# Optimization experiments

Hardware: AMD Instinct MI355X
Metric: run time of the kernel (lower is better)

## Reference

```python
import jax, jax.numpy as jnp
import numpy as np

CAPACITY_FACTOR = 2  # GShard top-2 gating: C = 2*S/E


def setup_inputs() -> dict:
    key = jax.random.key(0)
    k1, k2, k3, k4 = jax.random.split(key, 4)
    B, T, M, E, F = 4, 1024, 1024, 8, 4096
    x = jax.random.normal(k1, (B, T, M), dtype=jnp.float32)
    wg = jax.random.normal(k2, (M, E), dtype=jnp.float32) * 0.02
    w1 = jax.random.normal(k3, (E, M, F), dtype=jnp.float32) * 0.02
    w2 = jax.random.normal(k4, (E, F, M), dtype=jnp.float32) * 0.02
    return {"x": x, "wg": wg, "w1": w1, "w2": w2}


def top2_gate(xs, wg):
    # xs: [S, M] tokens; wg: [M, E] gate projection.
    S = xs.shape[0]
    E = wg.shape[1]
    C = CAPACITY_FACTOR * S // E  # expert capacity
    logits = xs @ wg                                  # [S, E]
    gates = jax.nn.softmax(logits, axis=-1)           # [S, E]
    # top-1 expert
    idx1 = jnp.argmax(gates, axis=-1)                 # [S]
    mask1 = jax.nn.one_hot(idx1, E, dtype=jnp.int32)  # [S, E]
    # top-2 expert: mask out top-1 and take argmax again
    logits_no1 = jnp.where(mask1.astype(bool), -jnp.inf, logits)
    idx2 = jnp.argmax(logits_no1, axis=-1)
    mask2 = jax.nn.one_hot(idx2, E, dtype=jnp.int32)
    # positions within each expert's buffer (cumsum over tokens)
    loc1 = jnp.cumsum(mask1, axis=0) - 1              # [S, E]
    loc2 = jnp.cumsum(mask2, axis=0) - 1 + jnp.sum(mask1, axis=0, keepdims=True)
    # load-balancing auxiliary loss
    me = jnp.mean(gates, axis=0)
    ce = jnp.mean(mask1.astype(gates.dtype), axis=0)
    l_aux = jnp.mean(me * ce) * (E * E)
    # drop tokens beyond capacity
    mask1 = mask1 * (loc1 < C)
    mask2 = mask2 * (loc2 < C)
    loc1_s = jnp.sum(loc1 * mask1, axis=1)            # [S] slot of token in its top-1 expert
    loc2_s = jnp.sum(loc2 * mask2, axis=1)
    mask1f = mask1.astype(gates.dtype)
    mask2f = mask2.astype(gates.dtype)
    gates1_s = jnp.sum(gates * mask1f, axis=1)
    gates2_s = jnp.sum(gates * mask2f, axis=1)
    denom = gates1_s + gates2_s
    denom = jnp.where(denom < 1e-9, 1e-9, denom)
    g1 = gates1_s / denom
    g2 = gates2_s / denom
    # combine weights [S, E, C]
    combine = (g1[:, None] * mask1f)[:, :, None] * jax.nn.one_hot(loc1_s, C, dtype=gates.dtype)[:, None, :] \
            + (g2[:, None] * mask2f)[:, :, None] * jax.nn.one_hot(loc2_s, C, dtype=gates.dtype)[:, None, :]
    dispatch = (combine > 0).astype(gates.dtype)      # one-hot dispatch mask [S, E, C]
    return l_aux, combine, dispatch


def reference(x, wg, w1, w2):
    B, T, M = x.shape
    xs = x.reshape(-1, M)                                  # [S, M]
    l_aux, combine_weights, dispatch_mask = top2_gate(xs, wg)
    # dispatch: one-hot matmul (E*C x S) @ (S x M) -> [E, C, M]
    dispatched = jnp.einsum('sec,sm->ecm', dispatch_mask, xs)
    # per-expert FFN (relu)
    h = jax.nn.relu(jnp.einsum('ecm,emf->ecf', dispatched, w1))
    expert_out = jnp.einsum('ecf,efm->ecm', h, w2)         # [E, C, M]
    # combine: (S x E*C) @ (E*C x M) -> [S, M]
    combined = jnp.einsum('sec,ecm->sm', combine_weights, expert_out)
    return combined.reshape(B, T, M), l_aux
```

## Files before the change

### kernel.cpp

```cpp
#include <hip/hip_runtime.h>
#include <hip/hip_bf16.h>

typedef unsigned short u16;
typedef short bf16x8 __attribute__((ext_vector_type(8)));
typedef float f32x4 __attribute__((ext_vector_type(4)));
typedef u16 u16x8 __attribute__((ext_vector_type(8)));
typedef u16 u16x4 __attribute__((ext_vector_type(4)));

#define S_TOK 4096
#define MDIM 1024
#define EDIM 8
#define FDIM 4096
#define CCAP 1024
#define HALF_F 2048

__device__ __align__(16) u16   g_xb [S_TOK * MDIM];
__device__ __align__(16) u16   g_wT [EDIM * FDIM * MDIM];
__device__ __align__(16) u16   g_h  [EDIM * CCAP * FDIM];
__device__ __align__(16) float g_eo [2 * EDIM * CCAP * MDIM];
__device__ float g_gates[S_TOK * EDIM];
__device__ int   g_idx1[S_TOK], g_idx2[S_TOK];
__device__ int   g_loc1[S_TOK], g_loc2[S_TOK];
__device__ float g_tg1[S_TOK],  g_tg2[S_TOK];
__device__ int   g_ts1[S_TOK],  g_ts2[S_TOK];
__device__ int   g_slot[EDIM * CCAP];

__device__ __forceinline__ u16 f2bf(float f) {
    union { float f; unsigned u; } c; c.f = f;
    unsigned r = c.u + 0x7FFFu + ((c.u >> 16) & 1u);
    return (u16)(r >> 16);
}
__device__ __forceinline__ void async16(const void* g, void* l) {
    __builtin_amdgcn_global_load_lds(
        (const __attribute__((address_space(1))) unsigned int*)g,
        (__attribute__((address_space(3))) unsigned int*)l, 16, 0, 0);
}

__global__ void gate_kernel(const float* __restrict__ x, const float* __restrict__ wg) {
    __shared__ float wgT[EDIM * MDIM];
    const int tid = threadIdx.x, wave = tid >> 6, lane = tid & 63;
    for (int i = tid; i < EDIM * MDIM; i += 256) {
        int e = i >> 10, m = i & 1023;
        wgT[i] = wg[m * EDIM + e];
    }
    __syncthreads();
    const int s = blockIdx.x * 4 + wave;
    const float* xr = x + (size_t)s * MDIM;
    float lg[EDIM];
#pragma unroll
    for (int e = 0; e < EDIM; e++) lg[e] = 0.f;
#pragma unroll
    for (int j = 0; j < 4; j++) {
        int m0 = j * 256 + lane * 4;
        float4 xv = *(const float4*)(xr + m0);
        u16x4 xb;
        xb[0] = f2bf(xv.x); xb[1] = f2bf(xv.y); xb[2] = f2bf(xv.z); xb[3] = f2bf(xv.w);
        *(u16x4*)(g_xb + (size_t)s * MDIM + m0) = xb;
#pragma unroll
        for (int e = 0; e < EDIM; e++) {
            float4 wv = *(const float4*)(&wgT[e * MDIM + m0]);
            lg[e] += xv.x * wv.x + xv.y * wv.y + xv.z * wv.z + xv.w * wv.w;
        }
    }
#pragma unroll
    for (int e = 0; e < EDIM; e++) {
        float v = lg[e];
        for (int o = 32; o >= 1; o >>= 1) v += __shfl_xor(v, o);
        lg[e] = v;
    }
    if (lane == 0) {
        float mx = lg[0];
#pragma unroll
        for (int e = 1; e < EDIM; e++) mx = fmaxf(mx, lg[e]);
        float ex[EDIM], sum = 0.f;
#pragma unroll
        for (int e = 0; e < EDIM; e++) { ex[e] = expf(lg[e] - mx); sum += ex[e]; }
        int i1 = 0; float b1 = lg[0];
#pragma unroll
        for (int e = 1; e < EDIM; e++) if (lg[e] > b1) { b1 = lg[e]; i1 = e; }
        int i2 = -1; float b2 = -3.4e38f;
#pragma unroll
        for (int e = 0; e < EDIM; e++) if (e != i1 && lg[e] > b2) { b2 = lg[e]; i2 = e; }
        float inv = 1.f / sum;
#pragma unroll
        for (int e = 0; e < EDIM; e++) g_gates[s * EDIM + e] = ex[e] * inv;
        g_idx1[s] = i1; g_idx2[s] = i2;
    }
}

__global__ void scan_kernel(float* __restrict__ out_laux) {
    __shared__ float me_sh[EDIM];
    __shared__ int cnt_sh[EDIM];
    const int t = threadIdx.x, wave = t >> 6, lane = t & 63;
    if (t < EDIM) { me_sh[t] = 0.f; cnt_sh[t] = 0; }
    for (int i = t; i < EDIM * CCAP; i += 1024) g_slot[i] = -1;
    __syncthreads();
    float lm[EDIM]; int lc[EDIM];
#pragma unroll
    for (int e = 0; e < EDIM; e++) { lm[e] = 0.f; lc[e] = 0; }
    for (int j = 0; j < 4; j++) {
        int s = t + 1024 * j;
        const float* g = g_gates + (size_t)s * EDIM;
        int i1 = g_idx1[s];
#pragma unroll
        for (int e = 0; e < EDIM; e++) { lm[e] += g[e]; lc[e] += (i1 == e); }
    }
#pragma unroll
    for (int e = 0; e < EDIM; e++) {
        float v = lm[e]; int c = lc[e];
        for (int o = 32; o >= 1; o >>= 1) { v += __shfl_xor(v, o); c += __shfl_xor(c, o); }
        if (lane == 0) { atomicAdd(&me_sh[e], v); atomicAdd(&cnt_sh[e], c); }
    }
    __syncthreads();
    {
        int e = wave & 7;
        const int* idx = (wave < 8) ? g_idx1 : g_idx2;
        int* loc = (wave < 8) ? g_loc1 : g_loc2;
        int running = (wave < 8) ? 0 : cnt_sh[e];
        for (int s0 = 0; s0 < S_TOK; s0 += 64) {
            int v = idx[s0 + lane];
            bool f = (v == e);
            unsigned long long m = __ballot(f);
            int rank = __popcll(m & ((1ull << lane) - 1ull));
            if (f) loc[s0 + lane] = running + rank;
            running += __popcll(m);
        }
    }
    __syncthreads();
    for (int j = 0; j < 4; j++) {
        int s = t + 1024 * j;
        int e1 = g_idx1[s], e2 = g_idx2[s];
        int l1 = g_loc1[s], l2 = g_loc2[s];
        bool k1 = l1 < CCAP, k2 = l2 < CCAP;
        float G1 = k1 ? g_gates[s * EDIM + e1] : 0.f;
        float G2 = k2 ? g_gates[s * EDIM + e2] : 0.f;
        float den = G1 + G2; den = den < 1e-9f ? 1e-9f : den;
        g_tg1[s] = G1 / den; g_tg2[s] = G2 / den;
        g_ts1[s] = k1 ? (e1 * CCAP + l1) : -1;
        g_ts2[s] = k2 ? (e2 * CCAP + l2) : -1;
        if (k1) g_slot[e1 * CCAP + l1] = s;
        if (k2) g_slot[e2 * CCAP + l2] = s;
    }
    if (t == 0) {
        float la = 0.f;
        for (int e = 0; e < EDIM; e++)
            la += (me_sh[e] / (float)S_TOK) * ((float)cnt_sh[e] / (float)S_TOK);
        la *= (float)EDIM;
        out_laux[0] = la;
    }
}

template <int R, int C>
__global__ void transpose_cvt(const float* __restrict__ in) {
    __shared__ __align__(16) u16 t[64][72];
    const float* I = in + (size_t)blockIdx.z * R * C;
    u16* O = g_wT + (size_t)blockIdx.z * R * C;
    const int tid = threadIdx.x;
    const int c0 = blockIdx.x * 64, r0 = blockIdx.y * 64;
    const int rr = tid >> 4;
    const int cc = (tid & 15) * 4;
#pragma unroll
    for (int j = 0; j < 4; j++) {
        int r = rr + j * 16;
        float4 v = *(const float4*)(I + (size_t)(r0 + r) * C + c0 + cc);
        t[cc + 0][r] = f2bf(v.x);
        t[cc + 1][r] = f2bf(v.y);
        t[cc + 2][r] = f2bf(v.z);
        t[cc + 3][r] = f2bf(v.w);
    }
    __syncthreads();
    const int oc = tid >> 2;
    const int orr = (tid & 3) * 16;
    u16x8 a = *(const u16x8*)(&t[oc][orr]);
    u16x8 b = *(const u16x8*)(&t[oc][orr + 8]);
    u16* dst = O + (size_t)(c0 + oc) * R + r0 + orr;
    *(u16x8*)(dst) = a;
    *(u16x8*)(dst + 8) = b;
}

#define GSTAGE(pA, pB)                                                      \
    {                                                                       \
        async16(gA0, (pA) + stA0); async16(gA1, (pA) + stA1);               \
        async16(gB0, (pB) + stA0); async16(gB1, (pB) + stA1);               \
        gA0 += 32; gA1 += 32; gB0 += 32; gB1 += 32;                         \
    }

#define GCOMPUTE(pA, pB)                                                    \
    {                                                                       \
        bf16x8 af[4], bfr[4];                                               \
        _Pragma("unroll")                                                   \
        for (int i = 0; i < 4; i++) {                                       \
            af[i]  = *(const bf16x8*)((pA) + (wm + i * 16 + lrow) * 32 + cr);\
            bfr[i] = *(const bf16x8*)((pB) + (wn + i * 16 + lrow) * 32 + cr);\
        }                                                                   \
        __builtin_amdgcn_s_setprio(1);                                      \
        _Pragma("unroll")                                                   \
        for (int mi = 0; mi < 4; mi++)                                      \
            _Pragma("unroll")                                               \
            for (int ni = 0; ni < 4; ni++)                                  \
                acc[mi][ni] = __builtin_amdgcn_mfma_f32_16x16x32_bf16(      \
                    af[mi], bfr[ni], acc[mi][ni], 0, 0, 0);                 \
        __builtin_amdgcn_s_setprio(0);                                      \
    }

#define BAR __builtin_amdgcn_s_barrier()

#define GEMM_PIPELINE(T)                                                    \
    u16 *pa0 = As0, *pa1 = As1, *pa2 = As2;                                 \
    u16 *pb0 = Bs0, *pb1 = Bs1, *pb2 = Bs2;                                 \
    GSTAGE(pa0, pb0); GSTAGE(pa1, pb1); GSTAGE(pa2, pb2);                   \
    for (int t = 0; t < (T); ++t) {                                         \
        if (t < (T) - 2)       { asm volatile("s_waitcnt vmcnt(8)" ::: "memory"); } \
        else if (t == (T) - 2) { asm volatile("s_waitcnt vmcnt(4)" ::: "memory"); } \
        else                   { asm volatile("s_waitcnt vmcnt(0)" ::: "memory"); } \
        BAR;                                                                \
        GCOMPUTE(pa0, pb0);                                                 \
        BAR;                                                                \
        if (t + 3 < (T)) { GSTAGE(pa0, pb0); }                              \
        u16* tA = pa0; pa0 = pa1; pa1 = pa2; pa2 = tA;                      \
        u16* tB = pb0; pb0 = pb1; pb1 = pb2; pb2 = tB;                      \
    }

__global__ __launch_bounds__(256, 3) void gemm_gather() {
    __shared__ __align__(16) u16 As0[4096], As1[4096], As2[4096];
    __shared__ __align__(16) u16 Bs0[4096], Bs1[4096], Bs2[4096];
    const int tid = threadIdx.x, wave = tid >> 6, lane = tid & 63;
    const int id = (blockIdx.x & 7) * 256 + (blockIdx.x >> 3);
    const int by = id & 7, bx = (id >> 3) & 31, e = id >> 8;
    const int scol = (((lane & 3) ^ ((lane >> 3) & 3)) * 8);
    const int stA0 = wave * 512, stA1 = 2048 + wave * 512;
    const int sb = e * CCAP + by * 128;
    int s0 = g_slot[sb + wave * 16 + (lane >> 2)];      if (s0 < 0) s0 = 0;
    int s1 = g_slot[sb + 64 + wave * 16 + (lane >> 2)]; if (s1 < 0) s1 = 0;
    const u16* gA0 = g_xb + (size_t)s0 * MDIM + scol;
    const u16* gA1 = g_xb + (size_t)s1 * MDIM + scol;
    const u16* Bb = g_wT + ((size_t)e * FDIM + bx * 128) * MDIM;
    const u16* gB0 = Bb + (size_t)(wave * 16 + (lane >> 2)) * MDIM + scol;
    const u16* gB1 = gB0 + (size_t)64 * MDIM;

    f32x4 acc[4][4];
#pragma unroll
    for (int i = 0; i < 4; i++)
#pragma unroll
        for (int j = 0; j < 4; j++) { f32x4 z = {0.f, 0.f, 0.f, 0.f}; acc[i][j] = z; }
    const int wm = (wave >> 1) * 64, wn = (wave & 1) * 64;
    const int lrow = lane & 15, lq = lane >> 4;
    const int cr = ((lq ^ ((lrow >> 1) & 3)) * 8);

    GEMM_PIPELINE(MDIM / 32)

    const int r0 = by * 128 + wm + lq * 4;
    const int c0 = bx * 128 + wn + lrow;
    u16* D = g_h + (size_t)e * CCAP * FDIM;
#pragma unroll
    for (int mi = 0; mi < 4; mi++)
#pragma unroll
        for (int v = 0; v < 4; v++) {
            size_t r = (size_t)(r0 + mi * 16 + v) * FDIM;
#pragma unroll
            for (int ni = 0; ni < 4; ni++) {
                float xv = acc[mi][ni][v];
                xv = xv > 0.f ? xv : 0.f;
                D[r + c0 + ni * 16] = f2bf(xv);
            }
        }
}

__global__ __launch_bounds__(256, 3) void gemm_bt() {
    __shared__ __align__(16) u16 As0[4096], As1[4096], As2[4096];
    __shared__ __align__(16) u16 Bs0[4096], Bs1[4096], Bs2[4096];
    const int tid = threadIdx.x, wave = tid >> 6, lane = tid & 63;
    const int id = (blockIdx.x & 7) * 128 + (blockIdx.x >> 3);
    const int by = id & 7, bx = (id >> 3) & 7, z = id >> 6;
    const int e = z >> 1, ks = z & 1;
    const int scol = (((lane & 3) ^ ((lane >> 3) & 3)) * 8);
    const int stA0 = wave * 512, stA1 = 2048 + wave * 512;
    const u16* Ab = g_h + (size_t)e * CCAP * FDIM + (size_t)(by * 128) * FDIM + ks * HALF_F;
    const u16* Bb = g_wT + (size_t)e * MDIM * FDIM + (size_t)(bx * 128) * FDIM + ks * HALF_F;
    const u16* gA0 = Ab + (size_t)(wave * 16 + (lane >> 2)) * FDIM + scol;
    const u16* gA1 = gA0 + (size_t)64 * FDIM;
    const u16* gB0 = Bb + (size_t)(wave * 16 + (lane >> 2)) * FDIM + scol;
    const u16* gB1 = gB0 + (size_t)64 * FDIM;

    f32x4 acc[4][4];
#pragma unroll
    for (int i = 0; i < 4; i++)
#pragma unroll
        for (int j = 0; j < 4; j++) { f32x4 z2 = {0.f, 0.f, 0.f, 0.f}; acc[i][j] = z2; }
    const int wm = (wave >> 1) * 64, wn = (wave & 1) * 64;
    const int lrow = lane & 15, lq = lane >> 4;
    const int cr = ((lq ^ ((lrow >> 1) & 3)) * 8);

    GEMM_PIPELINE(HALF_F / 32)

    const int r0 = by * 128 + wm + lq * 4;
    const int c0 = bx * 128 + wn + lrow;
    float* D = g_eo + (size_t)ks * (EDIM * CCAP * MDIM) + (size_t)e * CCAP * MDIM;
#pragma unroll
    for (int mi = 0; mi < 4; mi++)
#pragma unroll
        for (int v = 0; v < 4; v++) {
            size_t r = (size_t)(r0 + mi * 16 + v) * MDIM;
#pragma unroll
            for (int ni = 0; ni < 4; ni++)
                D[r + c0 + ni * 16] = acc[mi][ni][v];
        }
}

__global__ void combine_kernel(float* __restrict__ out) {
    const int s = blockIdx.x, t = threadIdx.x;
    constexpr size_t HALF = (size_t)EDIM * CCAP * MDIM;
    float g1 = g_tg1[s], g2 = g_tg2[s];
    int p1 = g_ts1[s], p2 = g_ts2[s];
    float a0 = 0.f, a1 = 0.f, a2 = 0.f, a3 = 0.f;
    if (p1 >= 0) {
        float4 v = ((const float4*)(g_eo + (size_t)p1 * MDIM))[t];
        float4 w = ((const float4*)(g_eo + HALF + (size_t)p1 * MDIM))[t];
        a0 = g1 * (v.x + w.x); a1 = g1 * (v.y + w.y);
        a2 = g1 * (v.z + w.z); a3 = g1 * (v.w + w.w);
    }
    if (p2 >= 0) {
        float4 v = ((const float4*)(g_eo + (size_t)p2 * MDIM))[t];
        float4 w = ((const float4*)(g_eo + HALF + (size_t)p2 * MDIM))[t];
        a0 += g2 * (v.x + w.x); a1 += g2 * (v.y + w.y);
        a2 += g2 * (v.z + w.z); a3 += g2 * (v.w + w.w);
    }
    float4 o; o.x = a0; o.y = a1; o.z = a2; o.w = a3;
    ((float4*)out)[(size_t)s * 256 + t] = o;
}

extern "C" void kernel_launch(void* const* d_in, const int* in_sizes, int n_in,
                              void* d_out, int out_size, void* d_ws, size_t ws_size,
                              hipStream_t stream) {
    const float* x  = (const float*)d_in[0];
    const float* wg = (const float*)d_in[1];
    const float* w1 = (const float*)d_in[2];
    const float* w2 = (const float*)d_in[3];
    float* out = (float*)d_out;

    gate_kernel<<<dim3(S_TOK / 4), 256, 0, stream>>>(x, wg);
    scan_kernel<<<dim3(1), 1024, 0, stream>>>(out + 4194304);

    transpose_cvt<MDIM, FDIM><<<dim3(FDIM / 64, MDIM / 64, EDIM), 256, 0, stream>>>(w1);
    gemm_gather<<<dim3(2048), 256, 0, stream>>>();

    transpose_cvt<FDIM, MDIM><<<dim3(MDIM / 64, FDIM / 64, EDIM), 256, 0, stream>>>(w2);
    gemm_bt<<<dim3(1024), 256, 0, stream>>>();

    combine_kernel<<<dim3(S_TOK), 256, 0, stream>>>(out);
}
```

Measured before the change: 540.8 us.

## Switch expert GEMMs to 256x256 tiles with 8-wave blocks and split-phase pipeline

Both expert GEMMs move from 128x128 tiles on 4-wave blocks to 256x256 tiles on 8-wave, 512-thread blocks. Each wave now computes a 128x64 sub-tile in two half-steps, with global-to-LDS staging of A and B interleaved between the MFMA phases over a 3-stage buffer. The larger tiles double operand reuse per loaded byte. In exchange, the grids shrink to 512 and 256 blocks with one block per CU (launch_bounds 512,1), which risks poor occupancy and tail imbalance on 256 CUs, plus more barriers per k-step.

Result: faster. 504.9 us (-6.6%).

```diff
diff --git a/kernel.cpp b/kernel.cpp
--- a/kernel.cpp
+++ b/kernel.cpp
@@ -178,132 +178,139 @@
     *(u16x8*)(dst + 8) = b;
 }
 
-#define GSTAGE(pA, pB)                                                      \
-    {                                                                       \
-        async16(gA0, (pA) + stA0); async16(gA1, (pA) + stA1);               \
-        async16(gB0, (pB) + stA0); async16(gB1, (pB) + stA1);               \
-        gA0 += 32; gA1 += 32; gB0 += 32; gB1 += 32;                         \
-    }
-
-#define GCOMPUTE(pA, pB)                                                    \
-    {                                                                       \
-        bf16x8 af[4], bfr[4];                                               \
-        _Pragma("unroll")                                                   \
-        for (int i = 0; i < 4; i++) {                                       \
-            af[i]  = *(const bf16x8*)((pA) + (wm + i * 16 + lrow) * 32 + cr);\
-            bfr[i] = *(const bf16x8*)((pB) + (wn + i * 16 + lrow) * 32 + cr);\
-        }                                                                   \
-        __builtin_amdgcn_s_setprio(1);                                      \
-        _Pragma("unroll")                                                   \
-        for (int mi = 0; mi < 4; mi++)                                      \
-            _Pragma("unroll")                                               \
-            for (int ni = 0; ni < 4; ni++)                                  \
-                acc[mi][ni] = __builtin_amdgcn_mfma_f32_16x16x32_bf16(      \
-                    af[mi], bfr[ni], acc[mi][ni], 0, 0, 0);                 \
-        __builtin_amdgcn_s_setprio(0);                                      \
-    }
-
-#define BAR __builtin_amdgcn_s_barrier()
-
-#define GEMM_PIPELINE(T)                                                    \
-    u16 *pa0 = As0, *pa1 = As1, *pa2 = As2;                                 \
-    u16 *pb0 = Bs0, *pb1 = Bs1, *pb2 = Bs2;                                 \
-    GSTAGE(pa0, pb0); GSTAGE(pa1, pb1); GSTAGE(pa2, pb2);                   \
-    for (int t = 0; t < (T); ++t) {                                         \
-        if (t < (T) - 2)       { asm volatile("s_waitcnt vmcnt(8)" ::: "memory"); } \
-        else if (t == (T) - 2) { asm volatile("s_waitcnt vmcnt(4)" ::: "memory"); } \
-        else                   { asm volatile("s_waitcnt vmcnt(0)" ::: "memory"); } \
-        BAR;                                                                \
-        GCOMPUTE(pa0, pb0);                                                 \
-        BAR;                                                                \
-        if (t + 3 < (T)) { GSTAGE(pa0, pb0); }                              \
-        u16* tA = pa0; pa0 = pa1; pa1 = pa2; pa2 = tA;                      \
-        u16* tB = pb0; pb0 = pb1; pb1 = pb2; pb2 = tB;                      \
-    }
-
-__global__ __launch_bounds__(256, 3) void gemm_gather() {
-    __shared__ __align__(16) u16 As0[4096], As1[4096], As2[4096];
-    __shared__ __align__(16) u16 Bs0[4096], Bs1[4096], Bs2[4096];
-    const int tid = threadIdx.x, wave = tid >> 6, lane = tid & 63;
-    const int id = (blockIdx.x & 7) * 256 + (blockIdx.x >> 3);
-    const int by = id & 7, bx = (id >> 3) & 31, e = id >> 8;
-    const int scol = (((lane & 3) ^ ((lane >> 3) & 3)) * 8);
-    const int stA0 = wave * 512, stA1 = 2048 + wave * 512;
-    const int sb = e * CCAP + by * 128;
-    int s0 = g_slot[sb + wave * 16 + (lane >> 2)];      if (s0 < 0) s0 = 0;
-    int s1 = g_slot[sb + 64 + wave * 16 + (lane >> 2)]; if (s1 < 0) s1 = 0;
-    const u16* gA0 = g_xb + (size_t)s0 * MDIM + scol;
-    const u16* gA1 = g_xb + (size_t)s1 * MDIM + scol;
-    const u16* Bb = g_wT + ((size_t)e * FDIM + bx * 128) * MDIM;
-    const u16* gB0 = Bb + (size_t)(wave * 16 + (lane >> 2)) * MDIM + scol;
-    const u16* gB1 = gB0 + (size_t)64 * MDIM;
-
-    f32x4 acc[4][4];
-#pragma unroll
-    for (int i = 0; i < 4; i++)
-#pragma unroll
-        for (int j = 0; j < 4; j++) { f32x4 z = {0.f, 0.f, 0.f, 0.f}; acc[i][j] = z; }
-    const int wm = (wave >> 1) * 64, wn = (wave & 1) * 64;
+#define ST_A0(s) { async16(pA0, ldsA + (s)*8192 + wid*512);        pA0 += 32; }
+#define ST_A1(s) { async16(pA1, ldsA + (s)*8192 + 4096 + wid*512); pA1 += 32; }
+#define ST_B0(s) { async16(pB0, ldsB + (s)*8192 + wid*512);        pB0 += 32; }
+#define ST_B1(s) { async16(pB1, ldsB + (s)*8192 + 4096 + wid*512); pB1 += 32; }
+
+#define GEMM256_BODY(NT)                                                     \
+    f32x4 acc[8][4];                                                         \
+    _Pragma("unroll")                                                        \
+    for (int i = 0; i < 8; i++)                                              \
+        _Pragma("unroll")                                                    \
+        for (int j = 0; j < 4; j++) { f32x4 z = {0.f,0.f,0.f,0.f}; acc[i][j] = z; } \
+    ST_A0(0); ST_A1(0); ST_B0(0); ST_B1(0);                                  \
+    ST_A0(1); ST_A1(1); ST_B0(1); ST_B1(1);                                  \
+    asm volatile("s_waitcnt vmcnt(4)" ::: "memory");                         \
+    __builtin_amdgcn_s_barrier();                                            \
+    int s = 0;                                                               \
+    for (int u = 0; u < (NT); ++u) {                                         \
+        int ps = s + 2; if (ps >= 3) ps -= 3;                                \
+        const u16* A = ldsA + s * 8192;                                      \
+        const u16* B = ldsB + s * 8192;                                      \
+        bf16x8 af[4], bfr[4];                                                \
+        _Pragma("unroll")                                                    \
+        for (int i = 0; i < 4; i++)                                          \
+            af[i] = *(const bf16x8*)(A + (wr*128 + i*16 + lrow)*32 + cr);    \
+        _Pragma("unroll")                                                    \
+        for (int i = 0; i < 4; i++)                                          \
+            bfr[i] = *(const bf16x8*)(B + (wc*64 + i*16 + lrow)*32 + cr);    \
+        if (u + 2 < (NT)) { ST_A0(ps); ST_A1(ps); }                          \
+        __builtin_amdgcn_s_barrier();                                        \
+        asm volatile("s_waitcnt lgkmcnt(0)" ::: "memory");                   \
+        __builtin_amdgcn_sched_barrier(0);                                   \
+        __builtin_amdgcn_s_setprio(1);                                       \
+        _Pragma("unroll")                                                    \
+        for (int i = 0; i < 4; i++)                                          \
+            _Pragma("unroll")                                                \
+            for (int j = 0; j < 4; j++)                                      \
+                acc[i][j] = __builtin_amdgcn_mfma_f32_16x16x32_bf16(         \
+                    af[i], bfr[j], acc[i][j], 0, 0, 0);                      \
+        __builtin_amdgcn_s_setprio(0);                                       \
+        __builtin_amdgcn_s_barrier();                                        \
+        _Pragma("unroll")                                                    \
+        for (int i = 0; i < 4; i++)                                          \
+            af[i] = *(const bf16x8*)(A + (wr*128 + 64 + i*16 + lrow)*32 + cr);\
+        if (u + 2 < (NT)) { ST_B0(ps); ST_B1(ps); }                          \
+        __builtin_amdgcn_s_barrier();                                        \
+        asm volatile("s_waitcnt lgkmcnt(0)" ::: "memory");                   \
+        __builtin_amdgcn_sched_barrier(0);                                   \
+        __builtin_amdgcn_s_setprio(1);                                       \
+        _Pragma("unroll")                                                    \
+        for (int i = 0; i < 4; i++)                                          \
+            _Pragma("unroll")                                                \
+            for (int j = 0; j < 4; j++)                                      \
+                acc[4+i][j] = __builtin_amdgcn_mfma_f32_16x16x32_bf16(       \
+                    af[i], bfr[j], acc[4+i][j], 0, 0, 0);                    \
+        __builtin_amdgcn_s_setprio(0);                                       \
+        if (u + 2 < (NT))      { asm volatile("s_waitcnt vmcnt(4)" ::: "memory"); } \
+        else if (u + 1 < (NT)) { asm volatile("s_waitcnt vmcnt(0)" ::: "memory"); } \
+        __builtin_amdgcn_s_barrier();                                        \
+        s = s + 1; if (s == 3) s = 0;                                        \
+    }
+
+__global__ __launch_bounds__(512, 1) void gemm_gather() {
+    __shared__ __align__(16) u16 lds[49152];
+    u16* ldsA = lds;
+    u16* ldsB = lds + 24576;
+    const int tid = threadIdx.x, wid = tid >> 6, lane = tid & 63;
+    const int wr = wid >> 2, wc = wid & 3;
     const int lrow = lane & 15, lq = lane >> 4;
-    const int cr = ((lq ^ ((lrow >> 1) & 3)) * 8);
-
-    GEMM_PIPELINE(MDIM / 32)
-
-    const int r0 = by * 128 + wm + lq * 4;
-    const int c0 = bx * 128 + wn + lrow;
+    const int cr   = (lq ^ ((lrow >> 1) & 3)) * 8;
+    const int scol = ((lane & 3) ^ ((lane >> 3) & 3)) * 8;
+    const int srow = tid >> 2;
+    const int id = (blockIdx.x & 7) * 64 + (blockIdx.x >> 3);
+    const int by = id & 3, bx = (id >> 2) & 15, e = id >> 6;
+
+    const int sb = e * CCAP + by * 256;
+    int t0 = g_slot[sb + srow];        if (t0 < 0) t0 = 0;
+    int t1 = g_slot[sb + 128 + srow];  if (t1 < 0) t1 = 0;
+    const u16* pA0 = g_xb + (size_t)t0 * MDIM + scol;
+    const u16* pA1 = g_xb + (size_t)t1 * MDIM + scol;
+    const u16* pB0 = g_wT + ((size_t)e * FDIM + bx * 256 + srow) * MDIM + scol;
+    const u16* pB1 = pB0 + (size_t)128 * MDIM;
+
+    GEMM256_BODY(MDIM / 32)
+
+    const int r0 = by * 256 + wr * 128 + lq * 4;
+    const int c0 = bx * 256 + wc * 64 + lrow;
     u16* D = g_h + (size_t)e * CCAP * FDIM;
 #pragma unroll
-    for (int mi = 0; mi < 4; mi++)
+    for (int fm = 0; fm < 8; fm++)
 #pragma unroll
         for (int v = 0; v < 4; v++) {
-            size_t r = (size_t)(r0 + mi * 16 + v) * FDIM;
-#pragma unroll
-            for (int ni = 0; ni < 4; ni++) {
-                float xv = acc[mi][ni][v];
+            size_t r = (size_t)(r0 + fm * 16 + v) * FDIM;
+#pragma unroll
+            for (int fn = 0; fn < 4; fn++) {
+                float xv = acc[fm][fn][v];
                 xv = xv > 0.f ? xv : 0.f;
-                D[r + c0 + ni * 16] = f2bf(xv);
+                D[r + c0 + fn * 16] = f2bf(xv);
             }
         }
 }
 
-__global__ __launch_bounds__(256, 3) void gemm_bt() {
-    __shared__ __align__(16) u16 As0[4096], As1[4096], As2[4096];
-    __shared__ __align__(16) u16 Bs0[4096], Bs1[4096], Bs2[4096];
-    const int tid = threadIdx.x, wave = tid >> 6, lane = tid & 63;
-    const int id = (blockIdx.x & 7) * 128 + (blockIdx.x >> 3);
-    const int by = id & 7, bx = (id >> 3) & 7, z = id >> 6;
+__global__ __launch_bounds__(512, 1) void gemm_bt() {
+    __shared__ __align__(16) u16 lds[49152];
+    u16* ldsA = lds;
+    u16* ldsB = lds + 24576;
+    const int tid = threadIdx.x, wid = tid >> 6, lane = tid & 63;
+    const int wr = wid >> 2, wc = wid & 3;
+    const int lrow = lane & 15, lq = lane >> 4;
+    const int cr   = (lq ^ ((lrow >> 1) & 3)) * 8;
+    const int scol = ((lane & 3) ^ ((lane >> 3) & 3)) * 8;
+    const int srow = tid >> 2;
+    const int id = (blockIdx.x & 7) * 32 + (blockIdx.x >> 3);
+    const int by = id & 3, bx = (id >> 2) & 3, z = id >> 4;
     const int e = z >> 1, ks = z & 1;
-    const int scol = (((lane & 3) ^ ((lane >> 3) & 3)) * 8);
-    const int stA0 = wave * 512, stA1 = 2048 + wave * 512;
-    const u16* Ab = g_h + (size_t)e * CCAP * FDIM + (size_t)(by * 128) * FDIM + ks * HALF_F;
-    const u16* Bb = g_wT + (size_t)e * MDIM * FDIM + (size_t)(bx * 128) * FDIM + ks * HALF_F;
-    const u16* gA0 = Ab + (size_t)(wave * 16 + (lane >> 2)) * FDIM + scol;
-    const u16* gA1 = gA0 + (size_t)64 * FDIM;
-    const u16* gB0 = Bb + (size_t)(wave * 16 + (lane >> 2)) * FDIM + scol;
-    const u16* gB1 = gB0 + (size_t)64 * FDIM;
-
-    f32x4 acc[4][4];
-#pragma unroll
-    for (int i = 0; i < 4; i++)
-#pragma unroll
-        for (int j = 0; j < 4; j++) { f32x4 z2 = {0.f, 0.f, 0.f, 0.f}; acc[i][j] = z2; }
-    const int wm = (wave >> 1) * 64, wn = (wave & 1) * 64;
-    const int lrow = lane & 15, lq = lane >> 4;
-    const int cr = ((lq ^ ((lrow >> 1) & 3)) * 8);
-
-    GEMM_PIPELINE(HALF_F / 32)
-
-    const int r0 = by * 128 + wm + lq * 4;
-    const int c0 = bx * 128 + wn + lrow;
+
+    const u16* pA0 = g_h + ((size_t)e * CCAP + by * 256 + srow) * FDIM + ks * HALF_F + scol;
+    const u16* pA1 = pA0 + (size_t)128 * FDIM;
+    const u16* pB0 = g_wT + ((size_t)e * MDIM + bx * 256 + srow) * FDIM + ks * HALF_F + scol;
+    const u16* pB1 = pB0 + (size_t)128 * FDIM;
+
+    GEMM256_BODY(HALF_F / 32)
+
+    const int r0 = by * 256 + wr * 128 + lq * 4;
+    const int c0 = bx * 256 + wc * 64 + lrow;
     float* D = g_eo + (size_t)ks * (EDIM * CCAP * MDIM) + (size_t)e * CCAP * MDIM;
 #pragma unroll
-    for (int mi = 0; mi < 4; mi++)
+    for (int fm = 0; fm < 8; fm++)
 #pragma unroll
         for (int v = 0; v < 4; v++) {
-            size_t r = (size_t)(r0 + mi * 16 + v) * MDIM;
-#pragma unroll
-            for (int ni = 0; ni < 4; ni++)
-                D[r + c0 + ni * 16] = acc[mi][ni][v];
+            size_t r = (size_t)(r0 + fm * 16 + v) * MDIM;
+#pragma unroll
+            for (int fn = 0; fn < 4; fn++)
+                D[r + c0 + fn * 16] = acc[fm][fn][v];
         }
 }
 
@@ -342,10 +349,10 @@
     scan_kernel<<<dim3(1), 1024, 0, stream>>>(out + 4194304);
 
     transpose_cvt<MDIM, FDIM><<<dim3(FDIM / 64, MDIM / 64, EDIM), 256, 0, stream>>>(w1);
-    gemm_gather<<<dim3(2048), 256, 0, stream>>>();
+    gemm_gather<<<dim3(512), 512, 0, stream>>>();
 
     transpose_cvt<FDIM, MDIM><<<dim3(MDIM / 64, FDIM / 64, EDIM), 256, 0, stream>>>(w2);
-    gemm_bt<<<dim3(1024), 256, 0, stream>>>();
+    gemm_bt<<<dim3(256), 512, 0, stream>>>();
 
     combine_kernel<<<dim3(S_TOK), 256, 0, stream>>>(out);
 }
```
